# Kernel optimization log

Measured on AMD Instinct MI355X. Metric: run time of the kernel, lower is better.

Reference implementation:

```python
import jax, jax.numpy as jnp
import numpy as np

N_EMBD = 1024
N_HEADS = 16
HEAD_DIM = N_EMBD // N_HEADS  # 64
NUM_BUCKETS = 32
MAX_DISTANCE = 64


def _relative_position_bucket(relative_position):
    # bidirectional=False path from the torch source
    rp = jnp.maximum(-relative_position, 0)  # valid (non-positive) rel positions -> distance
    max_exact = NUM_BUCKETS // 2
    is_small = rp < max_exact
    rp_f = jnp.maximum(rp, 1).astype(jnp.float32)  # guard log(0); masked by where
    large = max_exact + (
        jnp.log(rp_f / max_exact) / np.log(MAX_DISTANCE / max_exact) * (NUM_BUCKETS - max_exact)
    ).astype(jnp.int32)
    large = jnp.minimum(large, NUM_BUCKETS - 1)
    return jnp.where(is_small, rp, large)


def setup_inputs() -> dict:
    key = jax.random.key(0)
    ks = jax.random.split(key, 10)
    B, S = 2, 2048
    std = 1.0 / np.sqrt(N_EMBD)
    inp = {
        "hidden_states": jax.random.normal(ks[0], (B, S, N_EMBD), dtype=jnp.float32),
        "Wq": jax.random.normal(ks[1], (N_EMBD, N_EMBD), dtype=jnp.float32) * std,
        "bq": jnp.zeros((N_EMBD,), jnp.float32),
        "Wk": jax.random.normal(ks[2], (N_EMBD, N_EMBD), dtype=jnp.float32) * std,
        "bk": jnp.zeros((N_EMBD,), jnp.float32),
        "Wv": jax.random.normal(ks[3], (N_EMBD, N_EMBD), dtype=jnp.float32) * std,
        "bv": jnp.zeros((N_EMBD,), jnp.float32),
        "Wo": jax.random.normal(ks[4], (N_EMBD, N_EMBD), dtype=jnp.float32) * std,
        "bo": jnp.zeros((N_EMBD,), jnp.float32),
        "rel_bias": jax.random.normal(ks[5], (NUM_BUCKETS, N_HEADS), dtype=jnp.float32) * 0.1,
    }
    return inp


def reference(hidden_states, Wq, bq, Wk, bk, Wv, bv, Wo, bo, rel_bias):
    B, S, _ = hidden_states.shape

    def shape(x):  # [B,S,E] -> [B,H,S,D]
        return x.reshape(B, S, N_HEADS, HEAD_DIM).transpose(0, 2, 1, 3)

    scale = 1.0 / np.sqrt(HEAD_DIM)
    q = shape(hidden_states @ Wq + bq)
    k = shape(hidden_states @ Wk + bk)
    v = shape(hidden_states @ Wv + bv)

    scores = jnp.einsum("bhqd,bhkd->bhqk", q * scale, k)

    ctx = jnp.arange(S)[:, None]
    mem = jnp.arange(S)[None, :]
    bucket = _relative_position_bucket(mem - ctx)  # [S,S] int
    # [S,S,H] -> [1,H,S,S]
    position_bias = rel_bias[bucket].transpose(2, 0, 1)[None]
    scores = scores + position_bias * 8.0  # note the *8 from the source

    attn = jax.nn.softmax(scores.astype(jnp.float32), axis=-1).astype(scores.dtype)
    ctx_out = jnp.einsum("bhqk,bhkd->bhqd", attn, v)
    ctx_out = ctx_out.transpose(0, 2, 1, 3).reshape(B, S, N_EMBD)
    return ctx_out @ Wo + bo
```

## Files before the change

### kernel.cpp

```cpp
#include <hip/hip_runtime.h>
#include <math.h>


#define SEQ 2048
#define EMB 1024
#define NH 16
#define HD 64
#define LOG2E 1.44269504088896340736f
#define MU (1u << 20)

typedef short v8s __attribute__((ext_vector_type(8)));
typedef float v4f __attribute__((ext_vector_type(4)));
typedef float v16f __attribute__((ext_vector_type(16)));
typedef unsigned int v4u __attribute__((ext_vector_type(4)));

__device__ __forceinline__ v4f mfma16(v8s a, v8s b, v4f c) {
  return __builtin_amdgcn_mfma_f32_16x16x32_bf16(a, b, c, 0, 0, 0);
}
__device__ __forceinline__ v16f mfma32(v8s a, v8s b, v16f c) {
  return __builtin_amdgcn_mfma_f32_32x32x16_bf16(a, b, c, 0, 0, 0);
}
__device__ __forceinline__ unsigned short bfh(float x) {
  unsigned u = __builtin_bit_cast(unsigned, x);
  return (unsigned short)((u + 0x7FFFu + ((u >> 16) & 1u)) >> 16);
}
__device__ __forceinline__ float bff(unsigned short h) {
  unsigned u = (unsigned)h << 16;
  return __builtin_bit_cast(float, u);
}
__device__ __forceinline__ int imin(int a, int b) { return a < b ? a : b; }
__device__ __forceinline__ unsigned pk2(float a, float b) {
  unsigned h;
  asm("v_cvt_pk_bf16_f32 %0, %1, %2" : "=v"(h) : "v"(a), "v"(b));
  return h;
}
__device__ __forceinline__ void split2(float a, float b, unsigned& uh, unsigned& ul) {
  const unsigned h = pk2(a, b);
  const float ra = __builtin_bit_cast(float, h << 16);
  const float rb = __builtin_bit_cast(float, h & 0xFFFF0000u);
  uh = h;
  ul = pk2(a - ra, b - rb);
}
typedef const __attribute__((address_space(1))) unsigned char* gp_t;
typedef __attribute__((address_space(3))) unsigned char* lp_t;
__device__ __forceinline__ void gload16(const void* g, void* l) {
  __builtin_amdgcn_global_load_lds((gp_t)g, (lp_t)l, 16, 0, 0);
}
__device__ __forceinline__ int skey(int x) {
  return ((x & 7) + ((x >> 3) & 3)) & 7;
}

__global__ __launch_bounds__(256) void prep_kernel(
    const float* __restrict__ hs, const float* __restrict__ Wq,
    const float* __restrict__ Wk, const float* __restrict__ Wv,
    const float* __restrict__ Wo, unsigned short* __restrict__ wsu) {
  __shared__ float T[64][68];
  const int t = threadIdx.x;
  const int z = blockIdx.z;
  if (z == 4) {
    unsigned short* ah = wsu + 32u * MU;
    const int base = (blockIdx.y * 16 + blockIdx.x) * 16384 + t * 4;
#pragma unroll
    for (int i = 0; i < 16; ++i) {
      const int idx = base + i * 1024;
      const float4 v = *(const float4*)(hs + idx);
      *(uint2*)&ah[idx] = make_uint2(pk2(v.x, v.y), pk2(v.z, v.w));
    }
    return;
  }
  const float* W = (z == 0) ? Wq : (z == 1) ? Wk : (z == 2) ? Wv : Wo;
  const float s = (z == 0) ? 0.125f * LOG2E : 1.0f;
  const bool wlo = (z == 0 || z == 3);
  unsigned short* WTh = wsu + (size_t)(40u + 2u * z) * MU;
  unsigned short* WTl = WTh + MU;
  const int n0 = blockIdx.x * 64, k0 = blockIdx.y * 64;
  const int r = t >> 2, cs = (t & 3) * 16;
#pragma unroll
  for (int i = 0; i < 4; ++i)
    *(float4*)&T[r][cs + i * 4] =
        *(const float4*)(W + (size_t)(k0 + r) * EMB + n0 + cs + i * 4);
  __syncthreads();
  unsigned short hb[16], lb[16];
#pragma unroll
  for (int i = 0; i < 16; i += 2) {
    const float a = T[cs + i][r] * s, b2 = T[cs + i + 1][r] * s;
    unsigned uh, ul = 0;
    if (wlo) split2(a, b2, uh, ul);
    else uh = pk2(a, b2);
    hb[i] = (unsigned short)(uh & 0xFFFFu);
    hb[i + 1] = (unsigned short)(uh >> 16);
    lb[i] = (unsigned short)(ul & 0xFFFFu);
    lb[i + 1] = (unsigned short)(ul >> 16);
  }
  const size_t go = (size_t)(n0 + r) * EMB + k0 + cs;
  *(v8s*)&WTh[go] = *(v8s*)&hb[0];
  *(v8s*)&WTh[go + 8] = *(v8s*)&hb[8];
  if (wlo) {
    *(v8s*)&WTl[go] = *(v8s*)&lb[0];
    *(v8s*)&WTl[go + 8] = *(v8s*)&lb[8];
  }
}

struct alignas(16) G2Smem {
  unsigned short Ah[128][32], Bh[128][32], Bl[128][32];
};

__device__ __forceinline__ void gemm128_bf(
    const unsigned short* __restrict__ Ah_g,
    const unsigned short* __restrict__ Bh_g,
    const unsigned short* __restrict__ Bl_g,
    int m0, int n0, G2Smem& S, v4f acc[4][4], const bool useBl) {
  const int t = threadIdx.x;
  const int l = t & 63, w = t >> 6;
  const int wm = (w >> 1) << 6, wn = (w & 1) << 6;
  const int lg = l >> 4, lc = l & 15;
  const int r0 = t >> 2;
  const int gl = (t & 3) ^ ((r0 >> 1) & 3);
  unsigned short* lba = &S.Ah[0][0] + w * 512;
  unsigned short* lbb = &S.Bh[0][0] + w * 512;
  unsigned short* lbl = &S.Bl[0][0] + w * 512;
  for (int k0 = 0; k0 < EMB; k0 += 32) {
    __syncthreads();
    {
      const size_t sa0 = (size_t)(m0 + r0) * EMB + k0 + gl * 8;
      const size_t sb0 = (size_t)(n0 + r0) * EMB + k0 + gl * 8;
      gload16(Ah_g + sa0, lba);
      gload16(Ah_g + sa0 + (size_t)64 * EMB, lba + 2048);
      gload16(Bh_g + sb0, lbb);
      gload16(Bh_g + sb0 + (size_t)64 * EMB, lbb + 2048);
      if (useBl) {
        gload16(Bl_g + sb0, lbl);
        gload16(Bl_g + sb0 + (size_t)64 * EMB, lbl + 2048);
      }
    }
    asm volatile("s_waitcnt vmcnt(0)" ::: "memory");
    __syncthreads();
    v8s ah[4], bh[4], bl[4];
#pragma unroll
    for (int r = 0; r < 4; ++r) {
      const int ra = wm + r * 16 + lc;
      ah[r] = *(const v8s*)&S.Ah[ra][(lg ^ ((ra >> 1) & 3)) * 8];
      const int rb = wn + r * 16 + lc;
      bh[r] = *(const v8s*)&S.Bh[rb][(lg ^ ((rb >> 1) & 3)) * 8];
      if (useBl) bl[r] = *(const v8s*)&S.Bl[rb][(lg ^ ((rb >> 1) & 3)) * 8];
    }
#pragma unroll
    for (int i = 0; i < 4; ++i)
#pragma unroll
      for (int j = 0; j < 4; ++j) {
        acc[i][j] = mfma16(ah[i], bh[j], acc[i][j]);
        if (useBl) acc[i][j] = mfma16(ah[i], bl[j], acc[i][j]);
      }
  }
  __syncthreads();
}

__global__ __launch_bounds__(256) void qkv_mfma(
    const float* __restrict__ bq, const float* __restrict__ bk,
    const float* __restrict__ bv, unsigned short* __restrict__ wsu) {
  __shared__ G2Smem S;
  const int mat = blockIdx.y >> 3;
  const int m0 = blockIdx.x << 7, n0 = (blockIdx.y & 7) << 7;
  const unsigned short* Ah_g = wsu + 32u * MU;
  const unsigned short* Bh_g = wsu + (size_t)(40u + 2u * mat) * MU;
  const unsigned short* Bl_g = Bh_g + MU;
  const float* bias = (mat == 0) ? bq : (mat == 1) ? bk : bv;
  unsigned short* oh = wsu + (size_t)mat * 8u * MU;
  unsigned short* ol = oh + 4u * MU;

  v4f acc[4][4] = {};
  gemm128_bf(Ah_g, Bh_g, Bl_g, m0, n0, S, acc, mat == 0);

  const int t = threadIdx.x, l = t & 63, w = t >> 6;
  const int wm = (w >> 1) << 6, wn = (w & 1) << 6, lg = l >> 4, lc = l & 15;
  if (mat == 0) {
#pragma unroll
    for (int i = 0; i < 4; ++i)
#pragma unroll
      for (int j = 0; j < 4; ++j)
#pragma unroll
        for (int jr = 0; jr < 4; ++jr) {
          const int r = m0 + wm + i * 16 + lg * 4 + jr;
          const int cm = n0 + wn + j * 16 + lc;
          const float val = acc[i][j][jr] + bias[cm] * (0.125f * LOG2E);
          const unsigned short h = bfh(val);
          const size_t idx = (((size_t)((r >> 11) * NH + (cm >> 6)) * SEQ) +
                              (r & 2047)) * HD + (cm & 63);
          oh[idx] = h;
          ol[idx] = bfh(val - bff(h));
        }
  } else if (mat == 1) {
#pragma unroll
    for (int i = 0; i < 4; ++i)
#pragma unroll
      for (int j = 0; j < 4; ++j)
#pragma unroll
        for (int jr = 0; jr < 4; ++jr) {
          const int r = m0 + wm + i * 16 + lg * 4 + jr;
          const int cm = n0 + wn + j * 16 + lc;
          const float val = acc[i][j][jr] + bias[cm];
          const int s = r & 2047, d = cm & 63;
          const size_t idx = (((size_t)((r >> 11) * NH + (cm >> 6)) * SEQ) + s) * HD +
                             ((((d >> 3) ^ skey(s)) << 3) | (d & 7));
          oh[idx] = bfh(val);
        }
  } else {
    unsigned short* Traw = &S.Ah[0][0];
    unsigned short (*Th)[136] = (unsigned short(*)[136])Traw;
    const int b = m0 >> 11;
    const int s0base = m0 & 2047;
#pragma unroll
    for (int j = 0; j < 4; ++j) {
      __syncthreads();
#pragma unroll
      for (int i = 0; i < 4; ++i)
#pragma unroll
        for (int jr = 0; jr < 4; ++jr) {
          const int cm = n0 + wn + j * 16 + lc;
          const float val = acc[i][j][jr] + bias[cm];
          const int trow = (wn >> 2) + lc;
          const int tcol = wm + i * 16 + lg * 4 + jr;
          Th[trow][tcol] = bfh(val);
        }
      __syncthreads();
      const int tr = t >> 3, sgc = (t & 7) * 16;
      const int c = n0 + (tr >> 4) * 64 + j * 16 + (tr & 15);
      const int h2 = c >> 6, d = c & 63;
      const int sabs = s0base + sgc;
      const int g0 = (sabs >> 3) & 7;
      const size_t ob = ((size_t)(b * NH + h2) * HD + d) * SEQ + (sabs & ~63);
      const int o0 = (g0 ^ skey(d)) << 3, o1 = ((g0 + 1) ^ skey(d)) << 3;
      *(v8s*)&oh[ob + o0] = *(const v8s*)&Th[tr][sgc];
      *(v8s*)&oh[ob + o1] = *(const v8s*)&Th[tr][sgc + 8];
    }
  }
}

__device__ __forceinline__ v8s pfrag(unsigned a0, unsigned a1, unsigned a2,
                                     unsigned a3, int h5) {
  const unsigned sa = (unsigned)__shfl_xor((int)(h5 ? a0 : a2), 32, 64);
  const unsigned sb = (unsigned)__shfl_xor((int)(h5 ? a1 : a3), 32, 64);
  v4u r;
  r[0] = h5 ? sa : a0;
  r[1] = h5 ? sb : a1;
  r[2] = h5 ? a2 : sa;
  r[3] = h5 ? a3 : sb;
  return __builtin_bit_cast(v8s, r);
}

__global__ __launch_bounds__(256, 4) void attn_mfma(
    const float* __restrict__ rel_bias, unsigned short* __restrict__ wsu) {
  __shared__ struct alignas(16) {
    unsigned short Kh[2][64][64];
    unsigned short VTh[2][64][64];
    float bias8[32];
  } S;
  const int t = threadIdx.x;
  const int nid = (blockIdx.x & 7) * 128 + (blockIdx.x >> 3);
  const int half = nid >> 9;
  const int bh = (nid >> 4) & 31;
  const int qt = nid & 15;
  const int hh = bh & 15, b = bh >> 4;
  const int w = t >> 6, l = t & 63;
  const int lq = l & 31, h5 = l >> 5;
  const int qbase = qt * 128 + w * 32;
  const int kvbase = half << 10;
  const int kkey = skey(lq);

  const unsigned short* qh = wsu;
  const unsigned short* ql = wsu + 4u * MU;
  const unsigned short* kh = wsu + 8u * MU;
  const unsigned short* vth = wsu + 16u * MU;
  unsigned short* od = wsu + (half ? 28u : 24u) * MU;
  float2* stats = (float2*)(wsu + 36u * MU);

  if (t < 32) S.bias8[t] = rel_bias[t * NH + hh] * 8.0f * LOG2E;

  v8s qfh[4], qfl[4];
  const size_t qg = ((size_t)bh * SEQ + qbase + lq) * HD;
#pragma unroll
  for (int dc = 0; dc < 4; ++dc) {
    qfh[dc] = *(const v8s*)(qh + qg + dc * 16 + h5 * 8);
    qfl[dc] = *(const v8s*)(ql + qg + dc * 16 + h5 * 8);
  }

  float m_run = -1e30f, l_run = 0.0f;
  v16f acc[2] = {};

  const int srow = t >> 3, sg = t & 7;
  const size_t kbase_g = ((size_t)bh * SEQ + kvbase) * HD;
  const size_t vbase_g = (size_t)bh * HD * SEQ + kvbase;

  auto stage = [&](int kt, int bufsel) {
    const int kv0 = kt * 64;
    unsigned short* lk = &S.Kh[bufsel][0][0] + w * 512;
    unsigned short* lvh = &S.VTh[bufsel][0][0] + w * 512;
    gload16(kh + kbase_g + (size_t)(kv0 + srow) * HD + sg * 8, lk);
    gload16(kh + kbase_g + (size_t)(kv0 + srow + 32) * HD + sg * 8, lk + 2048);
    gload16(vth + vbase_g + (size_t)srow * SEQ + kv0 + sg * 8, lvh);
    gload16(vth + vbase_g + (size_t)(srow + 32) * SEQ + kv0 + sg * 8, lvh + 2048);
  };

  stage(0, 0);
  for (int kt = 0; kt < 16; ++kt) {
    const int buf = kt & 1;
    const int kv0 = kvbase + kt * 64;
    asm volatile("s_waitcnt vmcnt(0)" ::: "memory");
    __syncthreads();
    if (kt < 15) stage(kt + 1, buf ^ 1);

    v16f sc[2] = {};
    __builtin_amdgcn_s_setprio(1);
#pragma unroll
    for (int kb = 0; kb < 2; ++kb)
#pragma unroll
      for (int dc = 0; dc < 4; ++dc) {
        const int cswz = (((dc << 1) + h5) ^ kkey) << 3;
        const v8s kfh = *(const v8s*)&S.Kh[buf][kb * 32 + lq][cswz];
        sc[kb] = mfma32(kfh, qfh[dc], sc[kb]);
        sc[kb] = mfma32(kfh, qfl[dc], sc[kb]);
      }
    __builtin_amdgcn_s_setprio(0);

#pragma unroll
    for (int kb = 0; kb < 2; ++kb) {
      const int dq = qbase - (kv0 + kb * 32);
      if (dq + 31 <= 0) {
        const float bb = S.bias8[0];
#pragma unroll
        for (int r = 0; r < 16; ++r) sc[kb][r] += bb;
      } else if (dq >= 90) {
        const float bb = S.bias8[31];
#pragma unroll
        for (int r = 0; r < 16; ++r) sc[kb][r] += bb;
      } else {
#pragma unroll
        for (int r = 0; r < 16; ++r) {
          const int krow = (r & 3) + 8 * (r >> 2) + 4 * h5;
          int rp = (qbase + lq) - (kv0 + kb * 32 + krow);
          rp = rp > 0 ? rp : 0;
          const int bu =
              rp < 16 ? rp
                      : imin(16 + (int)(8.0f * __log2f((float)rp * 0.0625f)), 31);
          sc[kb][r] += S.bias8[bu];
        }
      }
    }

    float mt = sc[0][0];
#pragma unroll
    for (int r = 1; r < 16; ++r) mt = fmaxf(mt, sc[0][r]);
#pragma unroll
    for (int r = 0; r < 16; ++r) mt = fmaxf(mt, sc[1][r]);
    mt = fmaxf(mt, __shfl_xor(mt, 32, 64));
    if (__all(mt <= m_run + 8.0f) == 0) {
      const float mn = fmaxf(m_run, mt);
      const float fac = exp2f(m_run - mn);
      l_run *= fac;
#pragma unroll
      for (int r = 0; r < 16; ++r) {
        acc[0][r] *= fac;
        acc[1][r] *= fac;
      }
      m_run = mn;
    }
    unsigned pk[16];
    float rs = 0.0f;
#pragma unroll
    for (int i = 0; i < 16; ++i) {
      const float p0 = exp2f(sc[i >> 3][(2 * i) & 15] - m_run);
      const float p1 = exp2f(sc[i >> 3][(2 * i + 1) & 15] - m_run);
      rs += p0 + p1;
      pk[i] = pk2(p0, p1);
    }
    rs += __shfl_xor(rs, 32, 64);
    l_run += rs;

    __builtin_amdgcn_s_setprio(1);
#pragma unroll
    for (int ks = 0; ks < 4; ++ks) {
      const v8s pb = pfrag(pk[4 * ks], pk[4 * ks + 1], pk[4 * ks + 2],
                           pk[4 * ks + 3], h5);
      const int vswz = (((ks << 1) + h5) ^ kkey) << 3;
#pragma unroll
      for (int db = 0; db < 2; ++db) {
        const v8s vfh = *(const v8s*)&S.VTh[buf][db * 32 + lq][vswz];
        acc[db] = mfma32(vfh, pb, acc[db]);
      }
    }
    __builtin_amdgcn_s_setprio(0);
  }

  const float inv = 1.0f / l_run;
  const size_t rowb = ((size_t)b * SEQ + qbase + lq) * EMB + hh * HD;
#pragma unroll
  for (int db = 0; db < 2; ++db)
#pragma unroll
    for (int i = 0; i < 8; ++i) {
      const unsigned u = pk2(acc[db][2 * i] * inv, acc[db][2 * i + 1] * inv);
      const int d0 = db * 32 + 8 * (i >> 1) + 4 * h5 + 2 * (i & 1);
      *(unsigned*)&od[rowb + d0] = u;
    }
  if (h5 == 0)
    stats[(size_t)((half << 5) + bh) * SEQ + qbase + lq] =
        make_float2(m_run, l_run);
}

__global__ __launch_bounds__(256) void merge_kernel(unsigned short* __restrict__ wsu) {
  const int t = threadIdx.x;
  const size_t idx = ((size_t)blockIdx.x * 256 + t) * 16;
  const int row = (int)(idx >> 10);
  const int col = (int)(idx & 1023);
  const int b = row >> 11, s = row & 2047;
  const int bh = b * NH + (col >> 6);
  const float2* st = (const float2*)(wsu + 36u * MU);
  const float2 s0 = st[(size_t)bh * SEQ + s];
  const float2 s1 = st[(size_t)32 * SEQ + (size_t)bh * SEQ + s];
  const float M = fmaxf(s0.x, s1.x);
  const float w0 = s0.y * exp2f(s0.x - M);
  const float w1 = s1.y * exp2f(s1.x - M);
  const float inv = 1.0f / (w0 + w1);
  const float a0 = w0 * inv, a1 = w1 * inv;
  unsigned short* p0 = wsu + 24u * MU + idx;
  const unsigned short* p1 = wsu + 28u * MU + idx;
  const v8s x0a = *(const v8s*)p0, x0b = *(const v8s*)(p0 + 8);
  const v8s x1a = *(const v8s*)p1, x1b = *(const v8s*)(p1 + 8);
  unsigned short o[16];
#pragma unroll
  for (int e = 0; e < 8; ++e) {
    o[e] = bfh(a0 * bff((unsigned short)x0a[e]) + a1 * bff((unsigned short)x1a[e]));
    o[8 + e] =
        bfh(a0 * bff((unsigned short)x0b[e]) + a1 * bff((unsigned short)x1b[e]));
  }
  *(v8s*)p0 = *(const v8s*)&o[0];
  *(v8s*)(p0 + 8) = *(const v8s*)&o[8];
}

__global__ __launch_bounds__(256) void out_mfma(
    const float* __restrict__ bo, float* __restrict__ out,
    unsigned short* __restrict__ wsu) {
  __shared__ G2Smem S;
  const int m0 = blockIdx.x << 7, n0 = blockIdx.y << 7;
  const unsigned short* Ah_g = wsu + 24u * MU;
  const unsigned short* Bh_g = wsu + 46u * MU;
  const unsigned short* Bl_g = wsu + 47u * MU;
  v4f acc[4][4] = {};
  gemm128_bf(Ah_g, Bh_g, Bl_g, m0, n0, S, acc, true);
  const int t = threadIdx.x, l = t & 63, w = t >> 6;
  const int wm = (w >> 1) << 6, wn = (w & 1) << 6, lg = l >> 4, lc = l & 15;
#pragma unroll
  for (int i = 0; i < 4; ++i)
#pragma unroll
    for (int j = 0; j < 4; ++j)
#pragma unroll
      for (int jr = 0; jr < 4; ++jr) {
        const int r = m0 + wm + i * 16 + lg * 4 + jr;
        const int c = n0 + wn + j * 16 + lc;
        out[(size_t)r * EMB + c] = acc[i][j][jr] + bo[c];
      }
}

extern "C" void kernel_launch(void* const* d_in, const int* in_sizes, int n_in,
                              void* d_out, int out_size, void* d_ws, size_t ws_size,
                              hipStream_t stream) {
  const float* hs = (const float*)d_in[0];
  const float* Wq = (const float*)d_in[1];
  const float* bq = (const float*)d_in[2];
  const float* Wk = (const float*)d_in[3];
  const float* bk = (const float*)d_in[4];
  const float* Wv = (const float*)d_in[5];
  const float* bv = (const float*)d_in[6];
  const float* Wo = (const float*)d_in[7];
  const float* bo = (const float*)d_in[8];
  const float* rb = (const float*)d_in[9];
  unsigned short* wsu = (unsigned short*)d_ws;

  hipLaunchKernelGGL(prep_kernel, dim3(16, 16, 5), dim3(256), 0, stream,
                     hs, Wq, Wk, Wv, Wo, wsu);
  hipLaunchKernelGGL(qkv_mfma, dim3(32, 24), dim3(256), 0, stream, bq, bk, bv, wsu);
  hipLaunchKernelGGL(attn_mfma, dim3(1024), dim3(256), 0, stream, rb, wsu);
  hipLaunchKernelGGL(merge_kernel, dim3(1024), dim3(256), 0, stream, wsu);
  hipLaunchKernelGGL(out_mfma, dim3(32, 8), dim3(256), 0, stream, bo, (float*)d_out, wsu);
}
```

Before: 306.1 us.

## Store attention partials transposed, transpose in merge, drop Wo low split

The attention kernel now writes each split-KV partial output in a [bh][d][seq] layout, one bf16 per store, in place of the row-major context layout. The merge kernel combines the two halves per (head, 64-row tile) and transposes through shared memory into a separate context buffer. The output GEMM reads that buffer and drops the low-order bf16 correction term for Wo, which removes one MFMA pass at some cost in accuracy. The scalar 2-byte strided stores from attention may be less efficient than the previous packed stores.

```diff
diff --git a/kernel.cpp b/kernel.cpp
--- a/kernel.cpp
+++ b/kernel.cpp
@@ -70,7 +70,7 @@
   }
   const float* W = (z == 0) ? Wq : (z == 1) ? Wk : (z == 2) ? Wv : Wo;
   const float s = (z == 0) ? 0.125f * LOG2E : 1.0f;
-  const bool wlo = (z == 0 || z == 3);
+  const bool wlo = (z == 0);
   unsigned short* WTh = wsu + (size_t)(40u + 2u * z) * MU;
   unsigned short* WTl = WTh + MU;
   const int n0 = blockIdx.x * 64, k0 = blockIdx.y * 64;
@@ -260,7 +260,7 @@
   const int half = nid >> 9;
   const int bh = (nid >> 4) & 31;
   const int qt = nid & 15;
-  const int hh = bh & 15, b = bh >> 4;
+  const int hh = bh & 15;
   const int w = t >> 6, l = t & 63;
   const int lq = l & 31, h5 = l >> 5;
   const int qbase = qt * 128 + w * 32;
@@ -271,7 +271,7 @@
   const unsigned short* ql = wsu + 4u * MU;
   const unsigned short* kh = wsu + 8u * MU;
   const unsigned short* vth = wsu + 16u * MU;
-  unsigned short* od = wsu + (half ? 28u : 24u) * MU;
+  unsigned short* odT = wsu + (half ? 28u : 24u) * MU;
   float2* stats = (float2*)(wsu + 36u * MU);
 
   if (t < 32) S.bias8[t] = rel_bias[t * NH + hh] * 8.0f * LOG2E;
@@ -392,14 +392,13 @@
   }
 
   const float inv = 1.0f / l_run;
-  const size_t rowb = ((size_t)b * SEQ + qbase + lq) * EMB + hh * HD;
+  const size_t ob = (size_t)bh * HD * SEQ;
 #pragma unroll
   for (int db = 0; db < 2; ++db)
 #pragma unroll
-    for (int i = 0; i < 8; ++i) {
-      const unsigned u = pk2(acc[db][2 * i] * inv, acc[db][2 * i + 1] * inv);
-      const int d0 = db * 32 + 8 * (i >> 1) + 4 * h5 + 2 * (i & 1);
-      *(unsigned*)&od[rowb + d0] = u;
+    for (int r = 0; r < 16; ++r) {
+      const int d = db * 32 + (r & 3) + 8 * (r >> 2) + 4 * h5;
+      odT[ob + (size_t)d * SEQ + qbase + lq] = bfh(acc[db][r] * inv);
     }
   if (h5 == 0)
     stats[(size_t)((half << 5) + bh) * SEQ + qbase + lq] =
@@ -407,33 +406,43 @@
 }
 
 __global__ __launch_bounds__(256) void merge_kernel(unsigned short* __restrict__ wsu) {
+  __shared__ unsigned short T[64][72];
+  __shared__ float2 AB[64];
   const int t = threadIdx.x;
-  const size_t idx = ((size_t)blockIdx.x * 256 + t) * 16;
-  const int row = (int)(idx >> 10);
-  const int col = (int)(idx & 1023);
-  const int b = row >> 11, s = row & 2047;
-  const int bh = b * NH + (col >> 6);
+  const int s0 = blockIdx.x * 64;
+  const int bh = blockIdx.y;
+  const int b = bh >> 4, hh = bh & 15;
+  const unsigned short* o0 = wsu + 24u * MU;
+  const unsigned short* o1 = wsu + 28u * MU;
+  unsigned short* ctx = wsu + 32u * MU;
   const float2* st = (const float2*)(wsu + 36u * MU);
-  const float2 s0 = st[(size_t)bh * SEQ + s];
-  const float2 s1 = st[(size_t)32 * SEQ + (size_t)bh * SEQ + s];
-  const float M = fmaxf(s0.x, s1.x);
-  const float w0 = s0.y * exp2f(s0.x - M);
-  const float w1 = s1.y * exp2f(s1.x - M);
-  const float inv = 1.0f / (w0 + w1);
-  const float a0 = w0 * inv, a1 = w1 * inv;
-  unsigned short* p0 = wsu + 24u * MU + idx;
-  const unsigned short* p1 = wsu + 28u * MU + idx;
-  const v8s x0a = *(const v8s*)p0, x0b = *(const v8s*)(p0 + 8);
-  const v8s x1a = *(const v8s*)p1, x1b = *(const v8s*)(p1 + 8);
-  unsigned short o[16];
-#pragma unroll
-  for (int e = 0; e < 8; ++e) {
-    o[e] = bfh(a0 * bff((unsigned short)x0a[e]) + a1 * bff((unsigned short)x1a[e]));
-    o[8 + e] =
-        bfh(a0 * bff((unsigned short)x0b[e]) + a1 * bff((unsigned short)x1b[e]));
-  }
-  *(v8s*)p0 = *(const v8s*)&o[0];
-  *(v8s*)(p0 + 8) = *(const v8s*)&o[8];
+  if (t < 64) {
+    const float2 a = st[(size_t)bh * SEQ + s0 + t];
+    const float2 c = st[(size_t)(32 + bh) * SEQ + s0 + t];
+    const float M = fmaxf(a.x, c.x);
+    const float w0 = a.y * exp2f(a.x - M);
+    const float w1 = c.y * exp2f(c.x - M);
+    const float inv = 1.0f / (w0 + w1);
+    AB[t] = make_float2(w0 * inv, w1 * inv);
+  }
+  __syncthreads();
+  const int r = t >> 2, cs = (t & 3) * 16;
+  const size_t g = ((size_t)bh * HD + r) * SEQ + s0 + cs;
+  const v8s x0a = *(const v8s*)(o0 + g), x0b = *(const v8s*)(o0 + g + 8);
+  const v8s x1a = *(const v8s*)(o1 + g), x1b = *(const v8s*)(o1 + g + 8);
+#pragma unroll
+  for (int i = 0; i < 8; ++i) {
+    const float2 ab0 = AB[cs + i];
+    T[cs + i][r] = bfh(ab0.x * bff((unsigned short)x0a[i]) +
+                       ab0.y * bff((unsigned short)x1a[i]));
+    const float2 ab1 = AB[cs + 8 + i];
+    T[cs + 8 + i][r] = bfh(ab1.x * bff((unsigned short)x0b[i]) +
+                           ab1.y * bff((unsigned short)x1b[i]));
+  }
+  __syncthreads();
+  const size_t co = ((size_t)b * SEQ + s0 + r) * EMB + hh * HD + cs;
+  *(v8s*)&ctx[co] = *(const v8s*)&T[r][cs];
+  *(v8s*)&ctx[co + 8] = *(const v8s*)&T[r][cs + 8];
 }
 
 __global__ __launch_bounds__(256) void out_mfma(
@@ -441,11 +450,11 @@
     unsigned short* __restrict__ wsu) {
   __shared__ G2Smem S;
   const int m0 = blockIdx.x << 7, n0 = blockIdx.y << 7;
-  const unsigned short* Ah_g = wsu + 24u * MU;
+  const unsigned short* Ah_g = wsu + 32u * MU;
   const unsigned short* Bh_g = wsu + 46u * MU;
   const unsigned short* Bl_g = wsu + 47u * MU;
   v4f acc[4][4] = {};
-  gemm128_bf(Ah_g, Bh_g, Bl_g, m0, n0, S, acc, true);
+  gemm128_bf(Ah_g, Bh_g, Bl_g, m0, n0, S, acc, false);
   const int t = threadIdx.x, l = t & 63, w = t >> 6;
   const int wm = (w >> 1) << 6, wn = (w & 1) << 6, lg = l >> 4, lc = l & 15;
 #pragma unroll
@@ -479,6 +488,6 @@
                      hs, Wq, Wk, Wv, Wo, wsu);
   hipLaunchKernelGGL(qkv_mfma, dim3(32, 24), dim3(256), 0, stream, bq, bk, bv, wsu);
   hipLaunchKernelGGL(attn_mfma, dim3(1024), dim3(256), 0, stream, rb, wsu);
-  hipLaunchKernelGGL(merge_kernel, dim3(1024), dim3(256), 0, stream, wsu);
+  hipLaunchKernelGGL(merge_kernel, dim3(32, 32), dim3(256), 0, stream, wsu);
   hipLaunchKernelGGL(out_mfma, dim3(32, 8), dim3(256), 0, stream, bo, (float*)d_out, wsu);
 }
```

After: 290.8 us. 5.0% less time.
